# Performance work log

Hardware: AMD Instinct MI355X
Metric: run time of the kernel (lower is better)

## Reference

```python
import jax, jax.numpy as jnp
import numpy as np
from jax import lax

# minLSTM activation g(x) = x + 0.5 if x >= 0 else sigmoid(x)  (mingru repo functional.g)

def g_act(x):
    return jnp.where(x >= 0, x + 0.5, jax.nn.sigmoid(x))


def conv2d_seq(x5, w, b):
    # x5: (B,S,Cin,H,W), w: (Cout,Cin,3,3), stride 1, pad 1 -> (B,S,Cout,H,W)
    B, S = x5.shape[:2]
    xf = x5.reshape((B * S,) + x5.shape[2:])
    y = lax.conv_general_dilated(xf, w, window_strides=(1, 1),
                                 padding=[(1, 1), (1, 1)],
                                 dimension_numbers=("NCHW", "OIHW", "NCHW"))
    y = y + b[None, :, None, None]
    return y.reshape((B, S) + y.shape[1:])


def minlstm_layer(inp, w, b):
    # inp: (B,S,Cin,H,W) -> out h: (B,S,Cout,H,W)
    gates = conv2d_seq(inp, w, b)                     # (B,S,4C,H,W)
    i_g, f_g, o_g, cand = jnp.split(gates, 4, axis=2)  # each (B,S,C,H,W)
    it = jax.nn.sigmoid(i_g)
    ft = jax.nn.sigmoid(f_g)
    denom = it + ft
    fp = ft / denom                                   # normalized forget gate
    ig = (it / denom) * g_act(cand)                   # normalized input * candidate
    B, S, C, H, W = fp.shape
    # zero-init cell state passes through g: g(0) = 0.5 (init_hidden_state)
    c0 = jnp.full((B, C, H, W), 0.5, dtype=inp.dtype)

    def step(c, xs):
        fpt, igt = xs
        c_new = fpt * c + igt
        return c_new, c_new

    xs = (jnp.moveaxis(fp, 1, 0), jnp.moveaxis(ig, 1, 0))  # (S,B,C,H,W)
    _, cs = lax.scan(step, c0, xs)
    cs = jnp.moveaxis(cs, 0, 1)                       # (B,S,C,H,W)
    h = jax.nn.sigmoid(o_g) * cs                      # output gate
    return h


def setup_inputs() -> dict:
    key = jax.random.key(0)
    ks = jax.random.split(key, 5)
    x = jax.random.normal(ks[0], (4, 16, 32, 32, 32), dtype=jnp.float32)
    w0 = jax.random.normal(ks[1], (256, 32, 3, 3), dtype=jnp.float32) * 0.05
    b0 = jax.random.normal(ks[2], (256,), dtype=jnp.float32) * 0.05
    w1 = jax.random.normal(ks[3], (256, 64, 3, 3), dtype=jnp.float32) * 0.05
    b1 = jax.random.normal(ks[4], (256,), dtype=jnp.float32) * 0.05
    return {"x": x, "w0": w0, "b0": b0, "w1": w1, "b1": b1}


def reference(x, w0, b0, w1, b1):
    out = minlstm_layer(x, w0, b0)
    out = minlstm_layer(out, w1, b1)
    return out  # (B,S,64,H,W) — last layer outputs
```

## Files before the change

kernel.cpp:

```cpp
#include <hip/hip_runtime.h>


typedef __bf16 bf16x8 __attribute__((ext_vector_type(8)));
typedef float f32x4 __attribute__((ext_vector_type(4)));

#define N_IMG 64
#define HH 32
#define WW_ 32
#define HP 34
#define COUT 256

__device__ __forceinline__ float sigf(float x) { return 1.0f / (1.0f + __expf(-x)); }

__device__ __forceinline__ void gload16(void* lds, const void* g) {
  __builtin_amdgcn_global_load_lds(
      (const __attribute__((address_space(1))) void*)g,
      (__attribute__((address_space(3))) void*)lds, 16, 0, 0);
}

__global__ __launch_bounds__(256) void pack_x_k(const float* __restrict__ x,
                                                __bf16* __restrict__ xT) {
  __shared__ float ls[32][33];
  const int n = blockIdx.x >> 5;
  const int h = blockIdx.x & 31;
  const int t = threadIdx.x;
  {
    const int w = t & 31, g4 = t >> 5;
    const float* src = x + (((size_t)n * 32) << 10) + (h << 5);
#pragma unroll
    for (int j = 0; j < 4; ++j) {
      int ci = g4 * 4 + j;
      ls[ci][w] = src[((size_t)ci << 10) + w];
    }
  }
  __syncthreads();
  {
    const int ci = t & 31, w4 = t >> 5;
    __bf16* dst = xT + ((size_t)(n * HP + h + 1) * HP + 1) * 32 + ci;
#pragma unroll
    for (int j = 0; j < 4; ++j) {
      int w = w4 * 4 + j;
      dst[w * 32] = (__bf16)ls[ci][w];
    }
  }
}

template <int CIN>
__global__ __launch_bounds__(256) void pack_w_k(const float* __restrict__ w,
                                                __bf16* __restrict__ wT) {
  int g = blockIdx.x * 256 + threadIdx.x;
  if (g >= 256 * 9 * CIN) return;
  int co = g / (9 * CIN);
  int r = g - co * 9 * CIN;
  int khkw = r / CIN;
  int ci = r - khkw * CIN;
  wT[g] = (__bf16)w[(size_t)(co * CIN + ci) * 9 + khkw];
}

template <int CIN, bool LAYER1>
__global__ __launch_bounds__(256, 2) void conv_gemm_k(
    const __bf16* __restrict__ xT,
    const __bf16* __restrict__ wT,
    const float* __restrict__ bias,
    __bf16* __restrict__ gates) {
  constexpr int BK = CIN;
  constexpr int NKK = BK / 32;
  constexpr int CHUNKS = BK / 8;
  __shared__ bf16x8 lsA[CHUNKS * 128];
  __shared__ bf16x8 lsB[CHUNKS * 128];

  const int tid = threadIdx.x;
  const int lane = tid & 63;
  const int wid = tid >> 6;
  const int wr = wid >> 1, wc = wid & 1;

  const int bx = blockIdx.x;
  const int by = blockIdx.y;
  const int n = bx >> 3;
  const int h0 = (bx & 7) << 2;
  const int co0 = by << 7;

  f32x4 acc[4][4] = {};

  const size_t wrow = (size_t)9 * CIN;

  for (int t = 0; t < 9; ++t) {
    const int kh = t / 3;
    const int kw = t - kh * 3;
    for (int c = wid; c < 2 * CHUNKS; c += 4) {
      const int chunk = c >> 1;
      const int pix = ((c & 1) << 6) + lane;
      const int hh = h0 + (pix >> 5) + kh;
      const int ww = (pix & 31) + kw;
      const __bf16* src = xT + ((size_t)(n * HP + hh) * HP + ww) * CIN + chunk * 8;
      gload16((void*)(lsA + c * 64), (const void*)src);
    }
    for (int c = wid; c < 2 * CHUNKS; c += 4) {
      const int chunk = c >> 1;
      const int row = ((c & 1) << 6) + lane;
      const __bf16* src = wT + (size_t)(co0 + row) * wrow + t * CIN + chunk * 8;
      gload16((void*)(lsB + c * 64), (const void*)src);
    }
    __syncthreads();
#pragma unroll
    for (int kk = 0; kk < NKK; ++kk) {
      const int ca = kk * 4 + (lane >> 4);
      bf16x8 af[4], wf[4];
#pragma unroll
      for (int mi = 0; mi < 4; ++mi)
        af[mi] = lsA[ca * 128 + wr * 64 + mi * 16 + (lane & 15)];
#pragma unroll
      for (int ni = 0; ni < 4; ++ni)
        wf[ni] = lsB[ca * 128 + wc * 64 + ni * 16 + (lane & 15)];
#pragma unroll
      for (int mi = 0; mi < 4; ++mi)
#pragma unroll
        for (int ni = 0; ni < 4; ++ni) {
          if constexpr (!LAYER1)
            acc[mi][ni] = __builtin_amdgcn_mfma_f32_16x16x32_bf16(
                af[mi], wf[ni], acc[mi][ni], 0, 0, 0);
          else
            acc[mi][ni] = __builtin_amdgcn_mfma_f32_16x16x32_bf16(
                wf[ni], af[mi], acc[mi][ni], 0, 0, 0);
        }
    }
    __syncthreads();
  }

#pragma unroll
  for (int mi = 0; mi < 4; ++mi)
#pragma unroll
    for (int ni = 0; ni < 4; ++ni)
#pragma unroll
      for (int r = 0; r < 4; ++r) {
        if constexpr (!LAYER1) {
          const int m_loc = wr * 64 + mi * 16 + ((lane >> 4) << 2) + r;
          const int co = co0 + wc * 64 + ni * 16 + (lane & 15);
          const size_t m = (size_t)bx * 128 + m_loc;
          gates[m * 256 + co] = (__bf16)(acc[mi][ni][r] + bias[co]);
        } else {
          const int co = co0 + wc * 64 + ni * 16 + ((lane >> 4) << 2) + r;
          const int m_loc = wr * 64 + mi * 16 + (lane & 15);
          const int m = bx * 128 + m_loc;
          const int nimg = m >> 10, p = m & 1023;
          gates[((size_t)nimg * 256 + co) * 1024 + p] =
              (__bf16)(acc[mi][ni][r] + bias[co]);
        }
      }
}

__global__ __launch_bounds__(256) void scan0_k(const __bf16* __restrict__ gates,
                                               __bf16* __restrict__ h0T) {
  const int g = blockIdx.x * 256 + threadIdx.x;
  const int c = g & 63;
  const int p = (g >> 6) & 1023;
  const int b = g >> 16;
  const int h = p >> 5, w = p & 31;
  float cst = 0.5f;
#pragma unroll 4
  for (int s = 0; s < 16; ++s) {
    const size_t base = ((size_t)((b * 16 + s) * 1024 + p)) * 256 + c;
    const float ig_ = (float)gates[base];
    const float fg_ = (float)gates[base + 64];
    const float og_ = (float)gates[base + 128];
    const float cd_ = (float)gates[base + 192];
    const float it = sigf(ig_), ft = sigf(fg_);
    const float inv = 1.0f / (it + ft);
    const float gc = (cd_ >= 0.0f) ? (cd_ + 0.5f) : sigf(cd_);
    cst = (ft * inv) * cst + (it * inv) * gc;
    const float hv = sigf(og_) * cst;
    h0T[((size_t)((b * 16 + s) * HP + h + 1) * HP + (w + 1)) * 64 + c] =
        (__bf16)hv;
  }
}

__global__ __launch_bounds__(256) void scan1_k(const __bf16* __restrict__ gates,
                                               float* __restrict__ out) {
  const int g = blockIdx.x * 256 + threadIdx.x;
  const int p = g & 1023;
  const int c = (g >> 10) & 63;
  const int b = g >> 16;
  float cst = 0.5f;
#pragma unroll 4
  for (int s = 0; s < 16; ++s) {
    const size_t nb = (size_t)(b * 16 + s) * 256;
    const size_t base = (nb + c) * 1024 + p;
    const float ig_ = (float)gates[base];
    const float fg_ = (float)gates[base + 64 * 1024];
    const float og_ = (float)gates[base + 128 * 1024];
    const float cd_ = (float)gates[base + 192 * 1024];
    const float it = sigf(ig_), ft = sigf(fg_);
    const float inv = 1.0f / (it + ft);
    const float gc = (cd_ >= 0.0f) ? (cd_ + 0.5f) : sigf(cd_);
    cst = (ft * inv) * cst + (it * inv) * gc;
    const float hv = sigf(og_) * cst;
    out[((size_t)((b * 16 + s) * 64 + c)) * 1024 + p] = hv;
  }
}

extern "C" void kernel_launch(void* const* d_in, const int* in_sizes, int n_in,
                              void* d_out, int out_size, void* d_ws,
                              size_t ws_size, hipStream_t stream) {
  const float* x = (const float*)d_in[0];
  const float* w0 = (const float*)d_in[1];
  const float* b0 = (const float*)d_in[2];
  const float* w1 = (const float*)d_in[3];
  const float* b1 = (const float*)d_in[4];
  float* out = (float*)d_out;

  char* ws = (char*)d_ws;
  const size_t XT_BYTES = (size_t)N_IMG * HP * HP * 32 * 2;
  const size_t H0_BYTES = (size_t)N_IMG * HP * HP * 64 * 2;
  const size_t W0T_BYTES = (size_t)256 * 9 * 32 * 2;
  const size_t W1T_BYTES = (size_t)256 * 9 * 64 * 2;
  __bf16* xT = (__bf16*)ws;
  __bf16* h0T = (__bf16*)(ws + XT_BYTES);
  __bf16* w0T = (__bf16*)(ws + XT_BYTES + H0_BYTES);
  __bf16* w1T = (__bf16*)(ws + XT_BYTES + H0_BYTES + W0T_BYTES);
  __bf16* gates = (__bf16*)(ws + XT_BYTES + H0_BYTES + W0T_BYTES + W1T_BYTES);
  (void)ws_size; (void)n_in; (void)in_sizes; (void)out_size;

  hipMemsetAsync(xT, 0, XT_BYTES, stream);
  hipMemsetAsync(h0T, 0, H0_BYTES, stream);

  pack_x_k<<<N_IMG * 32, 256, 0, stream>>>(x, xT);
  pack_w_k<32><<<(256 * 9 * 32 + 255) / 256, 256, 0, stream>>>(w0, w0T);
  pack_w_k<64><<<(256 * 9 * 64 + 255) / 256, 256, 0, stream>>>(w1, w1T);

  conv_gemm_k<32, false><<<dim3(512, 2), 256, 0, stream>>>(xT, w0T, b0, gates);
  scan0_k<<<1024, 256, 0, stream>>>(gates, h0T);
  conv_gemm_k<64, true><<<dim3(512, 2), 256, 0, stream>>>(h0T, w1T, b1, gates);
  scan1_k<<<1024, 256, 0, stream>>>(gates, out);
}
```

Before: 177.4 us.

## Double-buffer conv GEMM LDS staging and vectorize scan kernels

Conv GEMM now double-buffers its LDS tiles so the async global->LDS loads for the next 3x3 tap are issued while MFMAs run on the current one. Layer 0 also gets higher occupancy launch bounds. Both scan kernels process 2 or 4 elements per thread with vector bf16 loads and vector stores, halving or quartering the grid. This cuts per-element load instructions and exposes memory-level parallelism. The cost is doubled LDS use and a single barrier per iteration, which relies on the global_load_lds writes being complete when the barrier is reached.

```diff
diff --git a/kernel.cpp b/kernel.cpp
--- a/kernel.cpp
+++ b/kernel.cpp
@@ -2,11 +2,11 @@
 
 
 typedef __bf16 bf16x8 __attribute__((ext_vector_type(8)));
+typedef __bf16 bf16x4 __attribute__((ext_vector_type(4)));
+typedef __bf16 bf16x2 __attribute__((ext_vector_type(2)));
 typedef float f32x4 __attribute__((ext_vector_type(4)));
 
 #define N_IMG 64
-#define HH 32
-#define WW_ 32
 #define HP 34
 #define COUT 256
 
@@ -58,16 +58,15 @@
 }
 
 template <int CIN, bool LAYER1>
-__global__ __launch_bounds__(256, 2) void conv_gemm_k(
+__global__ __launch_bounds__(256, LAYER1 ? 2 : 4) void conv_gemm_k(
     const __bf16* __restrict__ xT,
     const __bf16* __restrict__ wT,
     const float* __restrict__ bias,
     __bf16* __restrict__ gates) {
-  constexpr int BK = CIN;
-  constexpr int NKK = BK / 32;
-  constexpr int CHUNKS = BK / 8;
-  __shared__ bf16x8 lsA[CHUNKS * 128];
-  __shared__ bf16x8 lsB[CHUNKS * 128];
+  constexpr int NKK = CIN / 32;
+  constexpr int CHUNKS = CIN / 8;
+  __shared__ bf16x8 lsA[2][CHUNKS * 128];
+  __shared__ bf16x8 lsB[2][CHUNKS * 128];
 
   const int tid = threadIdx.x;
   const int lane = tid & 63;
@@ -81,37 +80,44 @@
   const int co0 = by << 7;
 
   f32x4 acc[4][4] = {};
-
   const size_t wrow = (size_t)9 * CIN;
 
-  for (int t = 0; t < 9; ++t) {
+  auto stage = [&](int buf, int t) {
     const int kh = t / 3;
     const int kw = t - kh * 3;
+#pragma unroll
     for (int c = wid; c < 2 * CHUNKS; c += 4) {
       const int chunk = c >> 1;
       const int pix = ((c & 1) << 6) + lane;
       const int hh = h0 + (pix >> 5) + kh;
       const int ww = (pix & 31) + kw;
-      const __bf16* src = xT + ((size_t)(n * HP + hh) * HP + ww) * CIN + chunk * 8;
-      gload16((void*)(lsA + c * 64), (const void*)src);
-    }
+      gload16((void*)(&lsA[buf][c * 64]),
+              (const void*)(xT + ((size_t)(n * HP + hh) * HP + ww) * CIN + chunk * 8));
+    }
+#pragma unroll
     for (int c = wid; c < 2 * CHUNKS; c += 4) {
       const int chunk = c >> 1;
       const int row = ((c & 1) << 6) + lane;
-      const __bf16* src = wT + (size_t)(co0 + row) * wrow + t * CIN + chunk * 8;
-      gload16((void*)(lsB + c * 64), (const void*)src);
-    }
-    __syncthreads();
+      gload16((void*)(&lsB[buf][c * 64]),
+              (const void*)(wT + (size_t)(co0 + row) * wrow + t * CIN + chunk * 8));
+    }
+  };
+
+  stage(0, 0);
+  __syncthreads();
+  int cur = 0;
+  for (int t = 0; t < 9; ++t) {
+    if (t < 8) stage(cur ^ 1, t + 1);
 #pragma unroll
     for (int kk = 0; kk < NKK; ++kk) {
       const int ca = kk * 4 + (lane >> 4);
       bf16x8 af[4], wf[4];
 #pragma unroll
       for (int mi = 0; mi < 4; ++mi)
-        af[mi] = lsA[ca * 128 + wr * 64 + mi * 16 + (lane & 15)];
+        af[mi] = lsA[cur][ca * 128 + wr * 64 + mi * 16 + (lane & 15)];
 #pragma unroll
       for (int ni = 0; ni < 4; ++ni)
-        wf[ni] = lsB[ca * 128 + wc * 64 + ni * 16 + (lane & 15)];
+        wf[ni] = lsB[cur][ca * 128 + wc * 64 + ni * 16 + (lane & 15)];
 #pragma unroll
       for (int mi = 0; mi < 4; ++mi)
 #pragma unroll
@@ -125,6 +131,7 @@
         }
     }
     __syncthreads();
+    cur ^= 1;
   }
 
 #pragma unroll
@@ -152,49 +159,58 @@
 __global__ __launch_bounds__(256) void scan0_k(const __bf16* __restrict__ gates,
                                                __bf16* __restrict__ h0T) {
   const int g = blockIdx.x * 256 + threadIdx.x;
-  const int c = g & 63;
-  const int p = (g >> 6) & 1023;
-  const int b = g >> 16;
+  const int c = (g & 31) * 2;
+  const int p = (g >> 5) & 1023;
+  const int b = g >> 15;
   const int h = p >> 5, w = p & 31;
-  float cst = 0.5f;
+  float c0 = 0.5f, c1 = 0.5f;
 #pragma unroll 4
   for (int s = 0; s < 16; ++s) {
     const size_t base = ((size_t)((b * 16 + s) * 1024 + p)) * 256 + c;
-    const float ig_ = (float)gates[base];
-    const float fg_ = (float)gates[base + 64];
-    const float og_ = (float)gates[base + 128];
-    const float cd_ = (float)gates[base + 192];
-    const float it = sigf(ig_), ft = sigf(fg_);
-    const float inv = 1.0f / (it + ft);
-    const float gc = (cd_ >= 0.0f) ? (cd_ + 0.5f) : sigf(cd_);
-    cst = (ft * inv) * cst + (it * inv) * gc;
-    const float hv = sigf(og_) * cst;
-    h0T[((size_t)((b * 16 + s) * HP + h + 1) * HP + (w + 1)) * 64 + c] =
-        (__bf16)hv;
+    const bf16x2* gp = reinterpret_cast<const bf16x2*>(gates + base);
+    const bf16x2 ig2 = gp[0], fg2 = gp[32], og2 = gp[64], cd2 = gp[96];
+    bf16x2 hv2;
+#pragma unroll
+    for (int j = 0; j < 2; ++j) {
+      const float it = sigf((float)ig2[j]), ft = sigf((float)fg2[j]);
+      const float inv = 1.0f / (it + ft);
+      const float cd_ = (float)cd2[j];
+      const float gc = (cd_ >= 0.0f) ? (cd_ + 0.5f) : sigf(cd_);
+      float& cst = j ? c1 : c0;
+      cst = (ft * inv) * cst + (it * inv) * gc;
+      hv2[j] = (__bf16)(sigf((float)og2[j]) * cst);
+    }
+    *reinterpret_cast<bf16x2*>(
+        h0T + ((size_t)((b * 16 + s) * HP + h + 1) * HP + (w + 1)) * 64 + c) = hv2;
   }
 }
 
 __global__ __launch_bounds__(256) void scan1_k(const __bf16* __restrict__ gates,
                                                float* __restrict__ out) {
   const int g = blockIdx.x * 256 + threadIdx.x;
-  const int p = g & 1023;
-  const int c = (g >> 10) & 63;
-  const int b = g >> 16;
-  float cst = 0.5f;
-#pragma unroll 4
+  const int p0 = (g & 255) * 4;
+  const int c = (g >> 8) & 63;
+  const int b = g >> 14;
+  float cst[4] = {0.5f, 0.5f, 0.5f, 0.5f};
+#pragma unroll 2
   for (int s = 0; s < 16; ++s) {
-    const size_t nb = (size_t)(b * 16 + s) * 256;
-    const size_t base = (nb + c) * 1024 + p;
-    const float ig_ = (float)gates[base];
-    const float fg_ = (float)gates[base + 64 * 1024];
-    const float og_ = (float)gates[base + 128 * 1024];
-    const float cd_ = (float)gates[base + 192 * 1024];
-    const float it = sigf(ig_), ft = sigf(fg_);
-    const float inv = 1.0f / (it + ft);
-    const float gc = (cd_ >= 0.0f) ? (cd_ + 0.5f) : sigf(cd_);
-    cst = (ft * inv) * cst + (it * inv) * gc;
-    const float hv = sigf(og_) * cst;
-    out[((size_t)((b * 16 + s) * 64 + c)) * 1024 + p] = hv;
+    const size_t base = ((size_t)(b * 16 + s) * 256 + c) * 1024 + p0;
+    const bf16x4 ig4 = *reinterpret_cast<const bf16x4*>(gates + base);
+    const bf16x4 fg4 = *reinterpret_cast<const bf16x4*>(gates + base + 64 * 1024);
+    const bf16x4 og4 = *reinterpret_cast<const bf16x4*>(gates + base + 128 * 1024);
+    const bf16x4 cd4 = *reinterpret_cast<const bf16x4*>(gates + base + 192 * 1024);
+    f32x4 hv;
+#pragma unroll
+    for (int j = 0; j < 4; ++j) {
+      const float it = sigf((float)ig4[j]), ft = sigf((float)fg4[j]);
+      const float inv = 1.0f / (it + ft);
+      const float cd_ = (float)cd4[j];
+      const float gc = (cd_ >= 0.0f) ? (cd_ + 0.5f) : sigf(cd_);
+      cst[j] = (ft * inv) * cst[j] + (it * inv) * gc;
+      hv[j] = sigf((float)og4[j]) * cst[j];
+    }
+    *reinterpret_cast<f32x4*>(
+        out + ((size_t)((b * 16 + s) * 64 + c)) * 1024 + p0) = hv;
   }
 }
 
@@ -228,7 +244,7 @@
   pack_w_k<64><<<(256 * 9 * 64 + 255) / 256, 256, 0, stream>>>(w1, w1T);
 
   conv_gemm_k<32, false><<<dim3(512, 2), 256, 0, stream>>>(xT, w0T, b0, gates);
-  scan0_k<<<1024, 256, 0, stream>>>(gates, h0T);
+  scan0_k<<<512, 256, 0, stream>>>(gates, h0T);
   conv_gemm_k<64, true><<<dim3(512, 2), 256, 0, stream>>>(h0T, w1T, b1, gates);
-  scan1_k<<<1024, 256, 0, stream>>>(gates, out);
-}
+  scan1_k<<<256, 256, 0, stream>>>(gates, out);
+}
```

Result: slower. 188.6 us (+6.3%).
